# Optimization experiments

Measured on AMD Instinct MI355X. Metric: run time of the kernel, lower is better.

Reference implementation:

```python
import jax, jax.numpy as jnp
import numpy as np

N_FFT = 1024
HOP = 256
WIN_LENGTH = 1024
B = 16
T = 480000


def setup_inputs() -> dict:
    key = jax.random.key(0)
    k1, k2 = jax.random.split(key)
    x = jax.random.normal(k1, (B, T), dtype=jnp.float32)
    window = jax.random.uniform(k2, (WIN_LENGTH,), dtype=jnp.float32)
    return {"x": x, "window": window}


def _dft_kernels(window):
    # pad window to n_fft if needed (here win_length == n_fft)
    if WIN_LENGTH < N_FFT:
        pl = (N_FFT - WIN_LENGTH) // 2
        window = jnp.pad(window, (pl, N_FFT - WIN_LENGTH - pl))
    n_freq = N_FFT // 2 + 1
    k = jnp.arange(n_freq, dtype=jnp.float32)[:, None]   # [F,1]
    n = jnp.arange(N_FFT, dtype=jnp.float32)[None, :]    # [1,N]
    basis = (2.0 * np.pi / N_FFT) * k * n                # [F,N]
    cos_k = jnp.cos(basis) * window[None, :]
    sin_k = -jnp.sin(basis) * window[None, :]
    return cos_k, sin_k


def reference(x, window):
    pad = N_FFT // 2
    xp = jnp.pad(x, ((0, 0), (pad, pad)), mode="reflect")  # center=True, reflect
    n_frames = (xp.shape[1] - N_FFT) // HOP + 1
    # frame extraction: [n_frames, n_fft] gather indices (strided windows)
    idx = jnp.arange(n_frames)[:, None] * HOP + jnp.arange(N_FFT)[None, :]
    frames = xp[:, idx]                                   # [B, n_frames, n_fft]
    cos_k, sin_k = _dft_kernels(window)                   # [F, n_fft]
    real = jnp.einsum("btn,fn->btf", frames, cos_k)        # [B, n_frames, F]
    imag = jnp.einsum("btn,fn->btf", frames, sin_k)
    return jnp.stack([real, imag], axis=-1)               # [B, n_frames, F, 2]
```

## Files before the change

### kernel.cpp

```cpp
#include <hip/hip_runtime.h>

#define BATCH     16
#define T_LEN     480000
#define PAD       512
#define TPAD      481024
#define HOP       256
#define NFFT      1024
#define NFRAMES   1876
#define M_TOTAL   30016
#define NOUTROW   1026
#define KTOT      1024

#define BM        128
#define BN        128
#define BK        32

typedef __attribute__((ext_vector_type(8))) short short8;
typedef __attribute__((ext_vector_type(4))) float floatx4;

__device__ __forceinline__ unsigned short f2bf(float f) {
  union { float f; unsigned int u; } v; v.f = f;
  unsigned int u = v.u;
  return (unsigned short)((u + 0x7FFFu + ((u >> 16) & 1u)) >> 16);
}
__device__ __forceinline__ float bf2f(unsigned short h) {
  union { unsigned int u; float f; } v; v.u = ((unsigned int)h) << 16;
  return v.f;
}

__global__ __launch_bounds__(256) void build_xp(const float* __restrict__ x,
                                                unsigned short* __restrict__ xp) {
  const int i = blockIdx.x * 256 + threadIdx.x;
  const int b = blockIdx.y;
  int j = i - PAD;
  if (j < 0) j = -j;
  if (j >= T_LEN) j = 2 * T_LEN - 2 - j;
  xp[(size_t)b * TPAD + i] = f2bf(x[(size_t)b * T_LEN + j]);
}

__global__ __launch_bounds__(256) void build_bmat(const float* __restrict__ win,
                                                  unsigned short* __restrict__ bm) {
  const int k = blockIdx.x * 256 + threadIdx.x;
  const int j = blockIdx.y;
  const int f = j >> 1;
  const int r = (f * k) & (NFFT - 1);
  const float ang = (float)r * 6.1359231515e-3f;
  const float c = __cosf(ang), s = __sinf(ang);
  const float v = (j & 1) ? -s : c;
  bm[(size_t)j * KTOT + k] = f2bf(v * win[k]);
}

__global__ __launch_bounds__(256) void stft_gemm(const unsigned short* __restrict__ xp,
                                                 const unsigned short* __restrict__ bmat,
                                                 float* __restrict__ out) {
  __shared__ unsigned short As[BM * BK];
  __shared__ unsigned short Bs[BN * BK];

  const int tid  = threadIdx.x;
  const int lane = tid & 63;
  const int wv   = tid >> 6;
  const int wr   = wv >> 1, wc = wv & 1;
  const int m0   = blockIdx.x * BM;
  const int j0   = blockIdx.y * BN;
  const int L    = lane & 15;
  const int quad = lane >> 4;

  const unsigned short* agsrc[2];
  const unsigned short* bgsrc[2];
#pragma unroll
  for (int p = 0; p < 2; ++p) {
    const int ci = p * 256 + tid;
    const int row = ci >> 2;
    const int c   = (ci & 3) ^ (row & 3);
    int gm = m0 + row; if (gm > M_TOTAL - 1) gm = M_TOTAL - 1;
    const int bb = gm / NFRAMES;
    const int tt = gm - bb * NFRAMES;
    agsrc[p] = xp   + (size_t)bb * TPAD + (size_t)tt * HOP + c * 8;
    bgsrc[p] = bmat + (size_t)(j0 + row) * KTOT + c * 8;
  }

  floatx4 acc[4][4] = {};

  for (int k0 = 0; k0 < KTOT; k0 += BK) {
#pragma unroll
    for (int p = 0; p < 2; ++p) {
      const int ci = p * 256 + tid;
      __builtin_amdgcn_global_load_lds(
          (const __attribute__((address_space(1))) void*)(agsrc[p] + k0),
          (__attribute__((address_space(3))) void*)((char*)As + ci * 16),
          16, 0, 0);
      __builtin_amdgcn_global_load_lds(
          (const __attribute__((address_space(1))) void*)(bgsrc[p] + k0),
          (__attribute__((address_space(3))) void*)((char*)Bs + ci * 16),
          16, 0, 0);
    }
    __syncthreads();

    short8 af[4], bfv[4];
#pragma unroll
    for (int t = 0; t < 4; ++t) {
      const int m = wr * 64 + t * 16 + L;
      const int ca = quad ^ (m & 3);
      af[t] = *(const short8*)&As[m * BK + ca * 8];
      const int n = wc * 64 + t * 16 + L;
      const int cb = quad ^ (n & 3);
      bfv[t] = *(const short8*)&Bs[n * BK + cb * 8];
    }
#pragma unroll
    for (int ti = 0; ti < 4; ++ti)
#pragma unroll
      for (int tj = 0; tj < 4; ++tj)
        acc[ti][tj] = __builtin_amdgcn_mfma_f32_16x16x32_bf16(
            af[ti], bfv[tj], acc[ti][tj], 0, 0, 0);
    __syncthreads();
  }

#pragma unroll
  for (int ti = 0; ti < 4; ++ti) {
    const int gmb = m0 + wr * 64 + ti * 16 + quad * 4;
#pragma unroll
    for (int tj = 0; tj < 4; ++tj) {
      const int gj = j0 + wc * 64 + tj * 16 + L;
#pragma unroll
      for (int i = 0; i < 4; ++i) {
        const int gm = gmb + i;
        if (gm < M_TOTAL) out[(size_t)gm * NOUTROW + gj] = acc[ti][tj][i];
      }
    }
  }
}

__global__ __launch_bounds__(256) void nyq_kernel(const unsigned short* __restrict__ xp,
                                                  const float* __restrict__ win,
                                                  float* __restrict__ out) {
  const int gwave = blockIdx.x * 4 + (threadIdx.x >> 6);
  const int lane  = threadIdx.x & 63;
  const int b = gwave / NFRAMES;
  const int t = gwave - b * NFRAMES;
  const unsigned short* src = xp + (size_t)b * TPAD + (size_t)t * HOP;
  float sum = 0.f;
#pragma unroll
  for (int i = 0; i < 4; ++i) {
    const int e0 = (i * 64 + lane) * 4;
    const ushort4 xv = *(const ushort4*)(src + e0);
    const float4  wv = *(const float4*)(win + e0);
    sum += wv.x * bf2f(xv.x) - wv.y * bf2f(xv.y)
         + wv.z * bf2f(xv.z) - wv.w * bf2f(xv.w);
  }
#pragma unroll
  for (int off = 32; off > 0; off >>= 1) sum += __shfl_down(sum, off);
  if (lane == 0) {
    out[(size_t)gwave * NOUTROW + 1024] = sum;
    out[(size_t)gwave * NOUTROW + 1025] = 0.f;
  }
}

extern "C" void kernel_launch(void* const* d_in, const int* in_sizes, int n_in,
                              void* d_out, int out_size, void* d_ws, size_t ws_size,
                              hipStream_t stream) {
  const float* x   = (const float*)d_in[0];
  const float* win = (const float*)d_in[1];
  float* out = (float*)d_out;

  unsigned short* xp   = (unsigned short*)d_ws;
  unsigned short* bmat = xp + (size_t)BATCH * TPAD;

  build_xp  <<<dim3(TPAD / 256, BATCH), 256, 0, stream>>>(x, xp);
  build_bmat<<<dim3(KTOT / 256, 1024),  256, 0, stream>>>(win, bmat);
  stft_gemm <<<dim3((M_TOTAL + BM - 1) / BM, 1024 / BN), 256, 0, stream>>>(xp, bmat, out);
  nyq_kernel<<<M_TOTAL / 4, 256, 0, stream>>>(xp, win, out);
}
```

Before: 268.8 us.

## Load overlapping frame window once into LDS and fold Nyquist bin into GEMM

```diff
diff --git a/kernel.cpp b/kernel.cpp
--- a/kernel.cpp
+++ b/kernel.cpp
@@ -5,15 +5,17 @@
 #define PAD       512
 #define TPAD      481024
 #define HOP       256
-#define NFFT      1024
 #define NFRAMES   1876
-#define M_TOTAL   30016
+#define FRPAD     1920
 #define NOUTROW   1026
 #define KTOT      1024
+#define NCOLS     1152
 
 #define BM        128
 #define BN        128
 #define BK        32
+#define ACH       4352
+#define XPSTRIDE  493568
 
 typedef __attribute__((ext_vector_type(8))) short short8;
 typedef __attribute__((ext_vector_type(4))) float floatx4;
@@ -23,60 +25,82 @@
   unsigned int u = v.u;
   return (unsigned short)((u + 0x7FFFu + ((u >> 16) & 1u)) >> 16);
 }
-__device__ __forceinline__ float bf2f(unsigned short h) {
-  union { unsigned int u; float f; } v; v.u = ((unsigned int)h) << 16;
-  return v.f;
-}
 
 __global__ __launch_bounds__(256) void build_xp(const float* __restrict__ x,
                                                 unsigned short* __restrict__ xp) {
   const int i = blockIdx.x * 256 + threadIdx.x;
   const int b = blockIdx.y;
-  int j = i - PAD;
-  if (j < 0) j = -j;
-  if (j >= T_LEN) j = 2 * T_LEN - 2 - j;
-  xp[(size_t)b * TPAD + i] = f2bf(x[(size_t)b * T_LEN + j]);
+  unsigned short v = 0;
+  if (i < TPAD) {
+    int j = i - PAD;
+    if (j < 0) j = -j;
+    if (j >= T_LEN) j = 2 * T_LEN - 2 - j;
+    v = f2bf(x[(size_t)b * T_LEN + j]);
+  }
+  xp[(size_t)b * XPSTRIDE + i] = v;
 }
 
 __global__ __launch_bounds__(256) void build_bmat(const float* __restrict__ win,
                                                   unsigned short* __restrict__ bm) {
   const int k = blockIdx.x * 256 + threadIdx.x;
   const int j = blockIdx.y;
-  const int f = j >> 1;
-  const int r = (f * k) & (NFFT - 1);
-  const float ang = (float)r * 6.1359231515e-3f;
-  const float c = __cosf(ang), s = __sinf(ang);
-  const float v = (j & 1) ? -s : c;
-  bm[(size_t)j * KTOT + k] = f2bf(v * win[k]);
+  unsigned short o = 0;
+  if (j < NOUTROW) {
+    const int f = j >> 1;
+    const int r = (f * k) & (KTOT - 1);
+    const float ang = (float)r * 6.1359231515e-3f;
+    const float c = __cosf(ang), s = __sinf(ang);
+    const float v = (j & 1) ? -s : c;
+    o = f2bf(v * win[k]);
+  }
+  bm[(size_t)j * KTOT + k] = o;
 }
 
-__global__ __launch_bounds__(256) void stft_gemm(const unsigned short* __restrict__ xp,
-                                                 const unsigned short* __restrict__ bmat,
-                                                 float* __restrict__ out) {
-  __shared__ unsigned short As[BM * BK];
+__global__ __launch_bounds__(256, 2) void stft_gemm(const unsigned short* __restrict__ xp,
+                                                    const unsigned short* __restrict__ bmat,
+                                                    float* __restrict__ out) {
+  __shared__ unsigned short As[ACH * 8];
   __shared__ unsigned short Bs[BN * BK];
 
   const int tid  = threadIdx.x;
   const int lane = tid & 63;
   const int wv   = tid >> 6;
   const int wr   = wv >> 1, wc = wv & 1;
-  const int m0   = blockIdx.x * BM;
+  const int bx   = blockIdx.x;
+  const int b    = bx / 15;
+  const int t0   = (bx - b * 15) * BM;
   const int j0   = blockIdx.y * BN;
   const int L    = lane & 15;
   const int quad = lane >> 4;
 
-  const unsigned short* agsrc[2];
-  const unsigned short* bgsrc[2];
+  const unsigned short* abase = xp + (size_t)b * XPSTRIDE + (size_t)t0 * HOP;
+
+#pragma unroll
+  for (int r = 0; r < ACH / 256; ++r) {
+    const int ci = r * 256 + tid;
+    const int s  = ci ^ ((ci >> 5) & 7);
+    __builtin_amdgcn_global_load_lds(
+        (const __attribute__((address_space(1))) void*)(abase + s * 8),
+        (__attribute__((address_space(3))) void*)((char*)As + ci * 16),
+        16, 0, 0);
+  }
+
+  const unsigned short* bsrc[2];
 #pragma unroll
   for (int p = 0; p < 2; ++p) {
-    const int ci = p * 256 + tid;
-    const int row = ci >> 2;
-    const int c   = (ci & 3) ^ (row & 3);
-    int gm = m0 + row; if (gm > M_TOTAL - 1) gm = M_TOTAL - 1;
-    const int bb = gm / NFRAMES;
-    const int tt = gm - bb * NFRAMES;
-    agsrc[p] = xp   + (size_t)bb * TPAD + (size_t)tt * HOP + c * 8;
-    bgsrc[p] = bmat + (size_t)(j0 + row) * KTOT + c * 8;
+    const int ci  = p * 256 + tid;
+    const int col = ci >> 2, c = ci & 3;
+    bsrc[p] = bmat + (size_t)(j0 + col) * KTOT + c * 8;
+  }
+
+  int sbase[4];
+  const unsigned short* blds[4];
+#pragma unroll
+  for (int t = 0; t < 4; ++t) {
+    const int ml = wr * 64 + t * 16 + L;
+    sbase[t] = 32 * ml + quad;
+    const int n = wc * 64 + t * 16 + L;
+    blds[t] = &Bs[n * BK + quad * 8];
   }
 
   floatx4 acc[4][4] = {};
@@ -86,72 +110,45 @@
     for (int p = 0; p < 2; ++p) {
       const int ci = p * 256 + tid;
       __builtin_amdgcn_global_load_lds(
-          (const __attribute__((address_space(1))) void*)(agsrc[p] + k0),
-          (__attribute__((address_space(3))) void*)((char*)As + ci * 16),
-          16, 0, 0);
-      __builtin_amdgcn_global_load_lds(
-          (const __attribute__((address_space(1))) void*)(bgsrc[p] + k0),
+          (const __attribute__((address_space(1))) void*)(bsrc[p] + k0),
           (__attribute__((address_space(3))) void*)((char*)Bs + ci * 16),
           16, 0, 0);
     }
     __syncthreads();
 
-    short8 af[4], bfv[4];
+    short8 af[4], bf[4];
+    const int kc = k0 >> 3;
 #pragma unroll
     for (int t = 0; t < 4; ++t) {
-      const int m = wr * 64 + t * 16 + L;
-      const int ca = quad ^ (m & 3);
-      af[t] = *(const short8*)&As[m * BK + ca * 8];
-      const int n = wc * 64 + t * 16 + L;
-      const int cb = quad ^ (n & 3);
-      bfv[t] = *(const short8*)&Bs[n * BK + cb * 8];
+      const int s = sbase[t] + kc;
+      const int p = s ^ ((s >> 5) & 7);
+      af[t] = *(const short8*)&As[p * 8];
+      bf[t] = *(const short8*)blds[t];
     }
 #pragma unroll
     for (int ti = 0; ti < 4; ++ti)
 #pragma unroll
       for (int tj = 0; tj < 4; ++tj)
         acc[ti][tj] = __builtin_amdgcn_mfma_f32_16x16x32_bf16(
-            af[ti], bfv[tj], acc[ti][tj], 0, 0, 0);
+            af[ti], bf[tj], acc[ti][tj], 0, 0, 0);
     __syncthreads();
   }
 
 #pragma unroll
   for (int ti = 0; ti < 4; ++ti) {
-    const int gmb = m0 + wr * 64 + ti * 16 + quad * 4;
+    const int tb = t0 + wr * 64 + ti * 16 + quad * 4;
 #pragma unroll
     for (int tj = 0; tj < 4; ++tj) {
       const int gj = j0 + wc * 64 + tj * 16 + L;
+      if (gj < NOUTROW) {
 #pragma unroll
-      for (int i = 0; i < 4; ++i) {
-        const int gm = gmb + i;
-        if (gm < M_TOTAL) out[(size_t)gm * NOUTROW + gj] = acc[ti][tj][i];
+        for (int i = 0; i < 4; ++i) {
+          const int t = tb + i;
+          if (t < NFRAMES)
+            out[(size_t)(b * NFRAMES + t) * NOUTROW + gj] = acc[ti][tj][i];
+        }
       }
     }
-  }
-}
-
-__global__ __launch_bounds__(256) void nyq_kernel(const unsigned short* __restrict__ xp,
-                                                  const float* __restrict__ win,
-                                                  float* __restrict__ out) {
-  const int gwave = blockIdx.x * 4 + (threadIdx.x >> 6);
-  const int lane  = threadIdx.x & 63;
-  const int b = gwave / NFRAMES;
-  const int t = gwave - b * NFRAMES;
-  const unsigned short* src = xp + (size_t)b * TPAD + (size_t)t * HOP;
-  float sum = 0.f;
-#pragma unroll
-  for (int i = 0; i < 4; ++i) {
-    const int e0 = (i * 64 + lane) * 4;
-    const ushort4 xv = *(const ushort4*)(src + e0);
-    const float4  wv = *(const float4*)(win + e0);
-    sum += wv.x * bf2f(xv.x) - wv.y * bf2f(xv.y)
-         + wv.z * bf2f(xv.z) - wv.w * bf2f(xv.w);
-  }
-#pragma unroll
-  for (int off = 32; off > 0; off >>= 1) sum += __shfl_down(sum, off);
-  if (lane == 0) {
-    out[(size_t)gwave * NOUTROW + 1024] = sum;
-    out[(size_t)gwave * NOUTROW + 1025] = 0.f;
   }
 }
 
@@ -163,10 +160,9 @@
   float* out = (float*)d_out;
 
   unsigned short* xp   = (unsigned short*)d_ws;
-  unsigned short* bmat = xp + (size_t)BATCH * TPAD;
+  unsigned short* bmat = xp + (size_t)BATCH * XPSTRIDE;
 
-  build_xp  <<<dim3(TPAD / 256, BATCH), 256, 0, stream>>>(x, xp);
-  build_bmat<<<dim3(KTOT / 256, 1024),  256, 0, stream>>>(win, bmat);
-  stft_gemm <<<dim3((M_TOTAL + BM - 1) / BM, 1024 / BN), 256, 0, stream>>>(xp, bmat, out);
-  nyq_kernel<<<M_TOTAL / 4, 256, 0, stream>>>(xp, win, out);
+  build_xp  <<<dim3(XPSTRIDE / 256, BATCH), 256, 0, stream>>>(x, xp);
+  build_bmat<<<dim3(KTOT / 256, NCOLS),     256, 0, stream>>>(win, bmat);
+  stft_gemm <<<dim3(BATCH * (FRPAD / BM), NCOLS / BN), 256, 0, stream>>>(xp, bmat, out);
 }
```

New measurement: 250.7 us. -6.7%, faster.
